# Performance work log

Hardware: AMD Instinct MI355X
Metric: run time of the kernel (lower is better)

Reference implementation:

```python
import jax, jax.numpy as jnp
import numpy as np
from jax import lax

B, T, V, E, H, K = 64, 512, 30000, 256, 256, 9


def setup_inputs() -> dict:
    key = jax.random.key(0)
    ks = jax.random.split(key, 15)
    s = 0.08
    return {
        "word_inputs": jax.random.randint(ks[0], (B, T), 0, V),
        "word_seq_lengths": jax.random.randint(ks[1], (B,), 1, T + 1),
        "seq_token_label": jax.random.randint(ks[2], (B, T), 0, K),
        "word_vec": jax.random.normal(ks[3], (V, E), jnp.float32) * s,
        "W_ih_f": jax.random.normal(ks[4], (4 * H, E), jnp.float32) * s,
        "W_hh_f": jax.random.normal(ks[5], (4 * H, H), jnp.float32) * s,
        "b_f": jax.random.normal(ks[6], (4 * H,), jnp.float32) * s,
        "W_ih_b": jax.random.normal(ks[7], (4 * H, E), jnp.float32) * s,
        "W_hh_b": jax.random.normal(ks[8], (4 * H, H), jnp.float32) * s,
        "b_b": jax.random.normal(ks[9], (4 * H,), jnp.float32) * s,
        "W_out": jax.random.normal(ks[10], (K, 2 * H), jnp.float32) * s,
        "b_out": jax.random.normal(ks[11], (K,), jnp.float32) * s,
        "start_trans": jax.random.normal(ks[12], (K,), jnp.float32) * s,
        "end_trans": jax.random.normal(ks[13], (K,), jnp.float32) * s,
        "trans": jax.random.normal(ks[14], (K, K), jnp.float32) * s,
    }


def _lstm_dir(x, W_ih, W_hh, b):
    # x: [B,T,E] -> h: [B,T,H]; torch gate order (i, f, g, o)
    gx = jnp.einsum('bte,ge->btg', x, W_ih) + b  # input projection hoisted out of scan
    h0 = jnp.zeros((x.shape[0], W_hh.shape[1]), x.dtype)

    def step(carry, g_t):
        h, c = carry
        g = g_t + h @ W_hh.T
        i, f, gg, o = jnp.split(g, 4, axis=-1)
        c = jax.nn.sigmoid(f) * c + jax.nn.sigmoid(i) * jnp.tanh(gg)
        h = jax.nn.sigmoid(o) * jnp.tanh(c)
        return (h, c), h

    _, hs = lax.scan(step, (h0, h0), jnp.swapaxes(gx, 0, 1))
    return jnp.swapaxes(hs, 0, 1)


def reference(word_inputs, word_seq_lengths, seq_token_label, word_vec,
              W_ih_f, W_hh_f, b_f, W_ih_b, W_hh_b, b_b,
              W_out, b_out, start_trans, end_trans, trans):
    t_idx = jnp.arange(T)
    mask = t_idx[None, :] < word_seq_lengths[:, None]  # [B,T] bool (pack_padded semantics)
    # index map that reverses the valid prefix of each sequence (involution)
    rev_idx = jnp.where(mask, word_seq_lengths[:, None] - 1 - t_idx[None, :], t_idx[None, :])

    emb = word_vec[word_inputs]  # [B,T,E]
    h_fwd = _lstm_dir(emb, W_ih_f, W_hh_f, b_f)
    emb_rev = jnp.take_along_axis(emb, rev_idx[:, :, None], axis=1)
    h_bwd = jnp.take_along_axis(_lstm_dir(emb_rev, W_ih_b, W_hh_b, b_b), rev_idx[:, :, None], axis=1)
    feats = jnp.concatenate([h_fwd, h_bwd], axis=-1) * mask[:, :, None]  # [B,T,2H]
    emissions = feats @ W_out.T + b_out  # [B,T,K]

    mf = mask.astype(emissions.dtype)
    # ---- CRF numerator (score of gold path) ----
    emit_sc = jnp.take_along_axis(emissions, seq_token_label[:, :, None], 2)[:, :, 0]  # [B,T]
    num = start_trans[seq_token_label[:, 0]] + emit_sc[:, 0]
    trans_sc = trans[seq_token_label[:, :-1], seq_token_label[:, 1:]]  # [B,T-1]
    num = num + jnp.sum((trans_sc + emit_sc[:, 1:]) * mf[:, 1:], axis=1)
    last_tags = jnp.take_along_axis(seq_token_label, (word_seq_lengths - 1)[:, None], 1)[:, 0]
    num = num + end_trans[last_tags]

    # ---- CRF log-partition (alpha recursion) ----
    em_t = jnp.swapaxes(emissions[:, 1:], 0, 1)  # [T-1,B,K]
    mk_t = jnp.swapaxes(mask[:, 1:], 0, 1)       # [T-1,B]
    score0 = start_trans[None, :] + emissions[:, 0]  # [B,K]

    def alpha_step(score, inp):
        e_t, m_t = inp
        nxt = jax.nn.logsumexp(score[:, :, None] + trans[None], axis=1) + e_t
        return jnp.where(m_t[:, None], nxt, score), None

    scoreZ, _ = lax.scan(alpha_step, score0, (em_t, mk_t))
    denom = jax.nn.logsumexp(scoreZ + end_trans[None, :], axis=1)
    ner_loss = -jnp.mean(num - denom)  # reduction='mean' over batch, negated

    # ---- Viterbi decode ----
    def vit_step(score, inp):
        e_t, m_t = inp
        tot = score[:, :, None] + trans[None]  # [B,K,K]
        best_prev = jnp.argmax(tot, axis=1)    # [B,K]
        nxt = jnp.max(tot, axis=1) + e_t
        return jnp.where(m_t[:, None], nxt, score), best_prev

    scoreV, hist = lax.scan(vit_step, score0, (em_t, mk_t))  # hist [T-1,B,K]
    best_last = jnp.argmax(scoreV + end_trans[None, :], axis=1)  # [B]

    def back_step(cur, inp):
        h_t, m_t = inp
        new = jnp.take_along_axis(h_t, cur[:, None], 1)[:, 0]
        cur = jnp.where(m_t, new, cur)
        return cur, cur

    _, preds_rev = lax.scan(back_step, best_last, (hist[::-1], mk_t[::-1]))  # [T-1,B]
    preds = jnp.concatenate([jnp.swapaxes(preds_rev[::-1], 0, 1), best_last[:, None]], axis=1)  # [B,T]
    preds = jnp.where(mask, preds, 0)

    return ner_loss, preds, feats
```

## Files before the change

kernel.cpp:

```cpp
#include <hip/hip_runtime.h>
#include <hip/hip_bf16.h>
#include <math.h>

#ifndef __has_builtin
#define __has_builtin(x) 0
#endif

typedef unsigned int uint;
typedef unsigned short ushort;
typedef _Float16 half2_t __attribute__((ext_vector_type(2)));


__device__ __forceinline__ float sigm(float x) {
    return __fdividef(1.0f, 1.0f + __expf(-x));
}
__device__ __forceinline__ float tanh_fast(float x) {
    float sg = __fdividef(1.0f, 1.0f + __expf(-2.0f * x));
    return sg + sg - 1.0f;
}
__device__ __forceinline__ float dot2f(uint w, uint h, float acc) {
#if __has_builtin(__builtin_amdgcn_fdot2)
    return __builtin_amdgcn_fdot2(__builtin_bit_cast(half2_t, w),
                                  __builtin_bit_cast(half2_t, h), acc, false);
#else
    half2_t a = __builtin_bit_cast(half2_t, w);
    half2_t b = __builtin_bit_cast(half2_t, h);
    return acc + (float)a.x * (float)b.x + (float)a.y * (float)b.y;
#endif
}

__global__ __launch_bounds__(256) void zero_kernel(float* __restrict__ out,
                                                   const int* __restrict__ lens) {
    int bid = blockIdx.x;
    if (bid < 65536) {
        int g = bid * 256 + threadIdx.x;
        int row = g >> 9;
        int t = row & 511;
        int b = row >> 9;
        if (t >= lens[b]) out[32769 + g] = 0.0f;
    } else if (bid < 65536 + 128) {
        int p = (bid - 65536) * 256 + threadIdx.x;
        out[1 + p] = 0.0f;
    } else if (threadIdx.x == 0) {
        out[0] = 0.0f;
    }
}

__global__ __launch_bounds__(256) void pack_kernel(const float* __restrict__ WF,
                                                   const float* __restrict__ WB,
                                                   uint* __restrict__ wregF,
                                                   uint* __restrict__ wregB,
                                                   uint* __restrict__ wldsF,
                                                   uint* __restrict__ wldsB) {
    int id = blockIdx.x * 256 + threadIdx.x;
    const float* W = WF; uint* wr = wregF; uint* wl = wldsF;
    if (id >= 131072) { id -= 131072; W = WB; wr = wregB; wl = wldsB; }
    int tl = id & 511;
    int x  = (id >> 9) & 1;
    int m  = id >> 10;
    int j = tl >> 1, s = tl & 1;
    int q = (s << 1) + x;
    float f0 = W[(((q << 8) + j) << 8) + 2 * m];
    float f1 = W[(((q << 8) + j) << 8) + 2 * m + 1];
    ushort u0 = __builtin_bit_cast(ushort, (_Float16)f0);
    ushort u1 = __builtin_bit_cast(ushort, (_Float16)f1);
    uint pk = (uint)u0 | ((uint)u1 << 16);
    if (m < 96) wr[((m << 1) + x) * 512 + tl];
    if (m < 96) wr[((m << 1) + x) * 512 + tl] = pk;
    else        wl[((m - 96) << 10) + (tl << 1) + x] = pk;
}

__global__ __launch_bounds__(256) void gemm_gx_kernel(const int* __restrict__ widx,
                                                      const int* __restrict__ lens,
                                                      const float* __restrict__ wvec,
                                                      const float* __restrict__ Wih,
                                                      const float* __restrict__ bias,
                                                      _Float16* __restrict__ gx) {
    int row0 = blockIdx.x * 64;
    int b = row0 >> 9;
    int t0 = row0 & 511;
    if (t0 >= lens[b]) return;
    int n0 = blockIdx.y * 64;

    __shared__ __align__(16) float As[16][68];
    __shared__ __align__(16) float Bs[16][68];
    __shared__ int aoff[64];

    int tid = threadIdx.x;
    if (tid < 64) aoff[tid] = widx[row0 + tid] << 8;
    __syncthreads();

    float acc[4][4] = {};
    int tn = tid & 15, tm = tid >> 4;

    for (int k0 = 0; k0 < 256; k0 += 16) {
#pragma unroll
        for (int p = 0; p < 4; ++p) {
            int lin = p * 256 + tid;
            int k = lin & 15, m = lin >> 4;
            int col = n0 + m;
            int perm = ((col & 3) << 8) + (col >> 2);
            As[k][m] = wvec[aoff[m] + k0 + k];
            Bs[k][m] = Wih[(perm << 8) + k0 + k];
        }
        __syncthreads();
#pragma unroll
        for (int k = 0; k < 16; ++k) {
            float4 av = *reinterpret_cast<const float4*>(&As[k][tm * 4]);
            float4 bv = *reinterpret_cast<const float4*>(&Bs[k][tn * 4]);
            float am[4] = {av.x, av.y, av.z, av.w};
            float bn[4] = {bv.x, bv.y, bv.z, bv.w};
#pragma unroll
            for (int i = 0; i < 4; ++i)
#pragma unroll
                for (int j = 0; j < 4; ++j) acc[i][j] = fmaf(am[i], bn[j], acc[i][j]);
        }
        __syncthreads();
    }

#pragma unroll
    for (int i = 0; i < 4; ++i) {
        int row = row0 + tm * 4 + i;
        ushort u[4];
#pragma unroll
        for (int j = 0; j < 4; ++j) {
            int col = n0 + tn * 4 + j;
            int perm = ((col & 3) << 8) + (col >> 2);
            u[j] = __builtin_bit_cast(ushort, (_Float16)(acc[i][j] + bias[perm]));
        }
        uint2 st;
        st.x = (uint)u[0] | ((uint)u[1] << 16);
        st.y = (uint)u[2] | ((uint)u[3] << 16);
        *reinterpret_cast<uint2*>(&gx[row * 1024 + n0 + tn * 4]) = st;
    }
}

__global__ __launch_bounds__(512, 2) void lstm_kernel(const _Float16* __restrict__ gx0,
                                                      const _Float16* __restrict__ gx1,
                                                      const uint* __restrict__ wreg0,
                                                      const uint* __restrict__ wreg1,
                                                      const uint* __restrict__ wlds0,
                                                      const uint* __restrict__ wlds1,
                                                      const int* __restrict__ lens,
                                                      float* __restrict__ feats) {
    int dir = blockIdx.x & 1;
    int b = blockIdx.x >> 1;
    const uint* gxu = reinterpret_cast<const uint*>(dir ? gx1 : gx0) + ((size_t)(b << 9) << 9);
    const uint* wreg = dir ? wreg1 : wreg0;
    const uint* wlds = dir ? wlds1 : wlds0;
    int len = lens[b];
    int tid = threadIdx.x;
    int lane = tid & 63;
    int sg = tid & 1;

    __shared__ __align__(16) uint lw[32 * 1024];
    __shared__ __align__(16) uint hpair[2][128];

    for (int i = tid; i < 32768; i += 512) lw[i] = wlds[i];

    uint wA[96], wB[96];
#pragma unroll
    for (int m = 0; m < 96; ++m) {
        wA[m] = wreg[((m << 1) + 0) * 512 + tid];
        wB[m] = wreg[((m << 1) + 1) * 512 + tid];
    }
    __syncthreads();

    float c = 0.0f;
    uint r0 = 0, r1 = 0;
    int pp = 0;

    int t0i = dir ? (len - 1) : 0;
    uint g = gxu[(t0i << 9) + tid];

    for (int tp = 0; tp < len; ++tp) {
        int t = dir ? (len - 1 - tp) : tp;
        int tnn = dir ? (len - 2 - tp) : (tp + 1);
        tnn = tnn < 0 ? 0 : (tnn >= len ? len - 1 : tnn);
        uint gnext = gxu[(tnn << 9) + tid];

        half2_t gv = __builtin_bit_cast(half2_t, g);
        float aA = (float)gv.x;
        float aB = (float)gv.y;

#pragma unroll
        for (int m = 0; m < 96; ++m) {
            uint hp = (uint)__builtin_amdgcn_readlane((int)(m < 64 ? r0 : r1), m & 63);
            aA = dot2f(wA[m], hp, aA);
            aB = dot2f(wB[m], hp, aB);
        }
#pragma unroll
        for (int i = 0; i < 32; ++i) {
            uint hp = (uint)__builtin_amdgcn_readlane((int)r1, 32 + i);
            uint2 w = reinterpret_cast<const uint2*>(lw)[(i << 9) + tid];
            aA = dot2f(w.x, hp, aA);
            aB = dot2f(w.y, hp, aB);
        }

        float y = sg ? aA + aA : aA;
        float sgm = __fdividef(1.0f, 1.0f + __expf(-y));
        float pA = sg ? sgm + sgm - 1.0f : sgm;
        float pB = sigm(aB);

        float oA = __shfl_xor(pA, 1);
        float oB = __shfl_xor(pB, 1);
        float si = sg ? oA : pA;
        float sf = sg ? oB : pB;
        float tg = sg ? pA : oA;
        float so = sg ? pB : oB;

        c = sf * c + si * tg;
        float h = so * tanh_fast(c);

        if (!sg) {
            reinterpret_cast<ushort*>(hpair[pp])[tid >> 1] =
                __builtin_bit_cast(ushort, (_Float16)h);
            feats[(size_t)(((b << 9) + t)) * 512 + (dir << 8) + (tid >> 1)] = h;
        }
        __syncthreads();
        r0 = hpair[pp][lane];
        r1 = hpair[pp][64 + lane];
        pp ^= 1;
        g = gnext;
    }
}

__global__ __launch_bounds__(64) void emis_kernel(const float* __restrict__ feats,
                                                  const float* __restrict__ Wout,
                                                  const float* __restrict__ bout,
                                                  const int* __restrict__ lens,
                                                  float* __restrict__ emis) {
    int r = blockIdx.x;
    int b = r >> 9, t = r & 511;
    if (t >= lens[b]) return;
    int lane = threadIdx.x;
    const float* fr = feats + (size_t)r * 512;
    float f[8];
#pragma unroll
    for (int i = 0; i < 8; ++i) f[i] = fr[i * 64 + lane];
#pragma unroll
    for (int k = 0; k < 9; ++k) {
        float p = 0.0f;
#pragma unroll
        for (int i = 0; i < 8; ++i) p = fmaf(f[i], Wout[k * 512 + i * 64 + lane], p);
#pragma unroll
        for (int off = 32; off; off >>= 1) p += __shfl_down(p, off);
        if (lane == 0) emis[r * 9 + k] = p + bout[k];
    }
}

__global__ __launch_bounds__(64) void crf_kernel(const float* __restrict__ emis,
                                                 const int* __restrict__ lens,
                                                 const int* __restrict__ labels,
                                                 const float* __restrict__ start_trans,
                                                 const float* __restrict__ end_trans,
                                                 const float* __restrict__ trans,
                                                 float* __restrict__ out) {
    int b = blockIdx.x;
    int len = lens[b];
    int lane = threadIdx.x;
    __shared__ float alpha[9], vit[9];
    __shared__ unsigned char hist[512 * 9];
    const float* eb = emis + b * 512 * 9;
    const int* lb = labels + b * 512;

    float tr[9];
    if (lane < 9) {
#pragma unroll
        for (int i = 0; i < 9; ++i) tr[i] = trans[i * 9 + lane];
        float s0 = start_trans[lane] + eb[lane];
        alpha[lane] = s0;
        vit[lane] = s0;
    }
    __syncthreads();

    for (int t = 1; t < len; ++t) {
        float na = 0.0f, nv = 0.0f;
        if (lane < 9) {
            float e = eb[t * 9 + lane];
            float a[9];
#pragma unroll
            for (int i = 0; i < 9; ++i) a[i] = alpha[i] + tr[i];
            float m = a[0];
#pragma unroll
            for (int i = 1; i < 9; ++i) m = fmaxf(m, a[i]);
            float s = 0.0f;
#pragma unroll
            for (int i = 0; i < 9; ++i) s += __expf(a[i] - m);
            na = m + __logf(s) + e;
            float bv = vit[0] + tr[0];
            int bi = 0;
#pragma unroll
            for (int i = 1; i < 9; ++i) {
                float x = vit[i] + tr[i];
                if (x > bv) { bv = x; bi = i; }
            }
            nv = bv + e;
            hist[t * 9 + lane] = (unsigned char)bi;
        }
        __syncthreads();
        if (lane < 9) { alpha[lane] = na; vit[lane] = nv; }
        __syncthreads();
    }

    float part = 0.0f;
    for (int t = 1 + lane; t < len; t += 64) {
        int yp = lb[t - 1], y = lb[t];
        part += trans[yp * 9 + y] + eb[t * 9 + y];
    }
#pragma unroll
    for (int off = 32; off; off >>= 1) part += __shfl_down(part, off);

    if (lane == 0) {
        int y0 = lb[0];
        float num = start_trans[y0] + eb[y0] + part + end_trans[lb[len - 1]];
        float m = alpha[0] + end_trans[0];
        for (int j = 1; j < 9; ++j) m = fmaxf(m, alpha[j] + end_trans[j]);
        float s = 0.0f;
        for (int j = 0; j < 9; ++j) s += __expf(alpha[j] + end_trans[j] - m);
        float denom = m + __logf(s);
        atomicAdd(out, (denom - num) * (1.0f / 64.0f));

        float bm = vit[0] + end_trans[0];
        int cur = 0;
        for (int j = 1; j < 9; ++j) {
            float x = vit[j] + end_trans[j];
            if (x > bm) { bm = x; cur = j; }
        }
        float* preds = out + 1 + b * 512;
        preds[len - 1] = (float)cur;
        for (int t = len - 1; t >= 1; --t) {
            cur = hist[t * 9 + cur];
            preds[t - 1] = (float)cur;
        }
    }
}

extern "C" void kernel_launch(void* const* d_in, const int* in_sizes, int n_in,
                              void* d_out, int out_size, void* d_ws, size_t ws_size,
                              hipStream_t stream) {
    const int* widx = (const int*)d_in[0];
    const int* lens = (const int*)d_in[1];
    const int* labels = (const int*)d_in[2];
    const float* wvec = (const float*)d_in[3];
    const float* WihF = (const float*)d_in[4];
    const float* WhhF = (const float*)d_in[5];
    const float* bF = (const float*)d_in[6];
    const float* WihB = (const float*)d_in[7];
    const float* WhhB = (const float*)d_in[8];
    const float* bB = (const float*)d_in[9];
    const float* Wout = (const float*)d_in[10];
    const float* bout = (const float*)d_in[11];
    const float* start_trans = (const float*)d_in[12];
    const float* end_trans = (const float*)d_in[13];
    const float* trans9 = (const float*)d_in[14];
    float* out = (float*)d_out;
    char* ws = (char*)d_ws;

    _Float16* gxF = (_Float16*)(ws);
    _Float16* gxB = (_Float16*)(ws + 67108864);
    uint* wregF   = (uint*)(ws + 134217728);
    uint* wregB   = (uint*)(ws + 134610944);
    uint* wldsF   = (uint*)(ws + 135004160);
    uint* wldsB   = (uint*)(ws + 135135232);
    float* emis   = (float*)(ws + 135266304);
    (void)in_sizes; (void)n_in; (void)out_size; (void)ws_size;

    float* feats = out + 1 + 32768;

    zero_kernel<<<65665, 256, 0, stream>>>(out, lens);
    pack_kernel<<<1024, 256, 0, stream>>>(WhhF, WhhB, wregF, wregB, wldsF, wldsB);

    dim3 ggrid(512, 16);
    gemm_gx_kernel<<<ggrid, 256, 0, stream>>>(widx, lens, wvec, WihF, bF, gxF);
    gemm_gx_kernel<<<ggrid, 256, 0, stream>>>(widx, lens, wvec, WihB, bB, gxB);

    lstm_kernel<<<128, 512, 0, stream>>>(gxF, gxB, wregF, wregB, wldsF, wldsB, lens, feats);

    emis_kernel<<<32768, 64, 0, stream>>>(feats, Wout, bout, lens, emis);
    crf_kernel<<<64, 64, 0, stream>>>(emis, lens, labels, start_trans, end_trans, trans9, out);
}
```

Measured before the change: 1.808 ms.

## Use fp16 dot2 in gx GEMM, rebalance LSTM register/LDS weight split

Pre-packs W_ih into fp16 pairs and rewrites the gx GEMM to accumulate with packed fp16 dot2 instructions. This halves the k-loop trips and the global loads per tile. In the LSTM recurrence, the register-resident weight columns drop from 96 to 90 and the LDS-resident part grows to 38 pairs. The LDS part is read with 128-bit loads covering two h pairs at once, which lowers register pressure and LDS instruction count. The risks are fp16 rounding of the embedding inputs in the GEMM and a wih16 workspace region that overlaps the emis buffer, though emis is written only after the GEMMs run.

```diff
diff --git a/kernel.cpp b/kernel.cpp
--- a/kernel.cpp
+++ b/kernel.cpp
@@ -10,6 +10,10 @@
 typedef unsigned short ushort;
 typedef _Float16 half2_t __attribute__((ext_vector_type(2)));
 
+#define PREG 90
+#define PLDS 38
+#define WREG_UINTS (PREG * 2 * 512)
+#define WLDS_UINTS (PLDS * 512 * 2)
 
 __device__ __forceinline__ float sigm(float x) {
     return __fdividef(1.0f, 1.0f + __expf(-x));
@@ -27,6 +31,11 @@
     half2_t b = __builtin_bit_cast(half2_t, h);
     return acc + (float)a.x * (float)b.x + (float)a.y * (float)b.y;
 #endif
+}
+__device__ __forceinline__ uint packh2(float a, float b) {
+    ushort u0 = __builtin_bit_cast(ushort, (_Float16)a);
+    ushort u1 = __builtin_bit_cast(ushort, (_Float16)b);
+    return (uint)u0 | ((uint)u1 << 16);
 }
 
 __global__ __launch_bounds__(256) void zero_kernel(float* __restrict__ out,
@@ -55,25 +64,48 @@
     int id = blockIdx.x * 256 + threadIdx.x;
     const float* W = WF; uint* wr = wregF; uint* wl = wldsF;
     if (id >= 131072) { id -= 131072; W = WB; wr = wregB; wl = wldsB; }
-    int tl = id & 511;
-    int x  = (id >> 9) & 1;
-    int m  = id >> 10;
+    int m, x, tl, dst_lds = 0, id2 = 0;
+    if (id < WREG_UINTS) {
+        m = id >> 10;
+        int r = id & 1023;
+        x = r >> 9;
+        tl = r & 511;
+    } else {
+        id2 = id - WREG_UINTS;
+        int c = id2 & 3;
+        int u = id2 >> 2;
+        tl = u & 511;
+        int g = u >> 9;
+        m = PREG + 2 * g + (c >> 1);
+        x = c & 1;
+        dst_lds = 1;
+    }
     int j = tl >> 1, s = tl & 1;
     int q = (s << 1) + x;
-    float f0 = W[(((q << 8) + j) << 8) + 2 * m];
-    float f1 = W[(((q << 8) + j) << 8) + 2 * m + 1];
-    ushort u0 = __builtin_bit_cast(ushort, (_Float16)f0);
-    ushort u1 = __builtin_bit_cast(ushort, (_Float16)f1);
-    uint pk = (uint)u0 | ((uint)u1 << 16);
-    if (m < 96) wr[((m << 1) + x) * 512 + tl];
-    if (m < 96) wr[((m << 1) + x) * 512 + tl] = pk;
-    else        wl[((m - 96) << 10) + (tl << 1) + x] = pk;
+    const float* row = W + ((size_t)((q << 8) + j) << 8);
+    uint pk = packh2(row[2 * m], row[2 * m + 1]);
+    if (dst_lds) wl[id2] = pk;
+    else         wr[((m << 1) + x) * 512 + tl] = pk;
+}
+
+__global__ __launch_bounds__(256) void wih_pack_kernel(const float* __restrict__ WihF,
+                                                       const float* __restrict__ WihB,
+                                                       uint* __restrict__ w16F,
+                                                       uint* __restrict__ w16B) {
+    int id = blockIdx.x * 256 + threadIdx.x;
+    const float* W = WihF; uint* dst = w16F;
+    if (id >= 131072) { id -= 131072; W = WihB; dst = w16B; }
+    int col = id >> 7;
+    int p = id & 127;
+    int perm = ((col & 3) << 8) + (col >> 2);
+    const float* row = W + ((size_t)perm << 8);
+    dst[(col << 7) + p] = packh2(row[2 * p], row[2 * p + 1]);
 }
 
 __global__ __launch_bounds__(256) void gemm_gx_kernel(const int* __restrict__ widx,
                                                       const int* __restrict__ lens,
                                                       const float* __restrict__ wvec,
-                                                      const float* __restrict__ Wih,
+                                                      const uint* __restrict__ wih16,
                                                       const float* __restrict__ bias,
                                                       _Float16* __restrict__ gx) {
     int row0 = blockIdx.x * 64;
@@ -82,8 +114,8 @@
     if (t0 >= lens[b]) return;
     int n0 = blockIdx.y * 64;
 
-    __shared__ __align__(16) float As[16][68];
-    __shared__ __align__(16) float Bs[16][68];
+    __shared__ __align__(16) uint As[16][68];
+    __shared__ __align__(16) uint Bs[16][68];
     __shared__ int aoff[64];
 
     int tid = threadIdx.x;
@@ -93,27 +125,27 @@
     float acc[4][4] = {};
     int tn = tid & 15, tm = tid >> 4;
 
-    for (int k0 = 0; k0 < 256; k0 += 16) {
+    for (int k0p = 0; k0p < 128; k0p += 16) {
 #pragma unroll
         for (int p = 0; p < 4; ++p) {
             int lin = p * 256 + tid;
-            int k = lin & 15, m = lin >> 4;
-            int col = n0 + m;
-            int perm = ((col & 3) << 8) + (col >> 2);
-            As[k][m] = wvec[aoff[m] + k0 + k];
-            Bs[k][m] = Wih[(perm << 8) + k0 + k];
+            int kp = lin & 15, m = lin >> 4;
+            const float2 av = *reinterpret_cast<const float2*>(
+                &wvec[aoff[m] + ((k0p + kp) << 1)]);
+            As[kp][m] = packh2(av.x, av.y);
+            Bs[kp][m] = wih16[((n0 + m) << 7) + k0p + kp];
         }
         __syncthreads();
 #pragma unroll
-        for (int k = 0; k < 16; ++k) {
-            float4 av = *reinterpret_cast<const float4*>(&As[k][tm * 4]);
-            float4 bv = *reinterpret_cast<const float4*>(&Bs[k][tn * 4]);
-            float am[4] = {av.x, av.y, av.z, av.w};
-            float bn[4] = {bv.x, bv.y, bv.z, bv.w};
+        for (int kp = 0; kp < 16; ++kp) {
+            uint4 a4 = *reinterpret_cast<const uint4*>(&As[kp][tm * 4]);
+            uint4 b4 = *reinterpret_cast<const uint4*>(&Bs[kp][tn * 4]);
+            uint am[4] = {a4.x, a4.y, a4.z, a4.w};
+            uint bn[4] = {b4.x, b4.y, b4.z, b4.w};
 #pragma unroll
             for (int i = 0; i < 4; ++i)
 #pragma unroll
-                for (int j = 0; j < 4; ++j) acc[i][j] = fmaf(am[i], bn[j], acc[i][j]);
+                for (int j = 0; j < 4; ++j) acc[i][j] = dot2f(am[i], bn[j], acc[i][j]);
         }
         __syncthreads();
     }
@@ -153,14 +185,14 @@
     int lane = tid & 63;
     int sg = tid & 1;
 
-    __shared__ __align__(16) uint lw[32 * 1024];
+    __shared__ __align__(16) uint lw[WLDS_UINTS];
     __shared__ __align__(16) uint hpair[2][128];
 
-    for (int i = tid; i < 32768; i += 512) lw[i] = wlds[i];
-
-    uint wA[96], wB[96];
-#pragma unroll
-    for (int m = 0; m < 96; ++m) {
+    for (int i = tid; i < WLDS_UINTS; i += 512) lw[i] = wlds[i];
+
+    uint wA[PREG], wB[PREG];
+#pragma unroll
+    for (int m = 0; m < PREG; ++m) {
         wA[m] = wreg[((m << 1) + 0) * 512 + tid];
         wB[m] = wreg[((m << 1) + 1) * 512 + tid];
     }
@@ -184,17 +216,20 @@
         float aB = (float)gv.y;
 
 #pragma unroll
-        for (int m = 0; m < 96; ++m) {
+        for (int m = 0; m < PREG; ++m) {
             uint hp = (uint)__builtin_amdgcn_readlane((int)(m < 64 ? r0 : r1), m & 63);
             aA = dot2f(wA[m], hp, aA);
             aB = dot2f(wB[m], hp, aB);
         }
 #pragma unroll
-        for (int i = 0; i < 32; ++i) {
-            uint hp = (uint)__builtin_amdgcn_readlane((int)r1, 32 + i);
-            uint2 w = reinterpret_cast<const uint2*>(lw)[(i << 9) + tid];
-            aA = dot2f(w.x, hp, aA);
-            aB = dot2f(w.y, hp, aB);
+        for (int i = 0; i < 19; ++i) {
+            uint4 w4 = reinterpret_cast<const uint4*>(lw)[(i << 9) + tid];
+            uint hp0 = (uint)__builtin_amdgcn_readlane((int)r1, 26 + 2 * i);
+            uint hp1 = (uint)__builtin_amdgcn_readlane((int)r1, 27 + 2 * i);
+            aA = dot2f(w4.x, hp0, aA);
+            aB = dot2f(w4.y, hp0, aB);
+            aA = dot2f(w4.z, hp1, aA);
+            aB = dot2f(w4.w, hp1, aB);
         }
 
         float y = sg ? aA + aA : aA;
@@ -360,9 +395,11 @@
     _Float16* gxF = (_Float16*)(ws);
     _Float16* gxB = (_Float16*)(ws + 67108864);
     uint* wregF   = (uint*)(ws + 134217728);
-    uint* wregB   = (uint*)(ws + 134610944);
-    uint* wldsF   = (uint*)(ws + 135004160);
-    uint* wldsB   = (uint*)(ws + 135135232);
+    uint* wregB   = (uint*)(ws + 134586368);
+    uint* wldsF   = (uint*)(ws + 134955008);
+    uint* wldsB   = (uint*)(ws + 135110656);
+    uint* wih16F  = (uint*)(ws + 135266304);
+    uint* wih16B  = (uint*)(ws + 135790592);
     float* emis   = (float*)(ws + 135266304);
     (void)in_sizes; (void)n_in; (void)out_size; (void)ws_size;
 
@@ -370,10 +407,11 @@
 
     zero_kernel<<<65665, 256, 0, stream>>>(out, lens);
     pack_kernel<<<1024, 256, 0, stream>>>(WhhF, WhhB, wregF, wregB, wldsF, wldsB);
+    wih_pack_kernel<<<1024, 256, 0, stream>>>(WihF, WihB, wih16F, wih16B);
 
     dim3 ggrid(512, 16);
-    gemm_gx_kernel<<<ggrid, 256, 0, stream>>>(widx, lens, wvec, WihF, bF, gxF);
-    gemm_gx_kernel<<<ggrid, 256, 0, stream>>>(widx, lens, wvec, WihB, bB, gxB);
+    gemm_gx_kernel<<<ggrid, 256, 0, stream>>>(widx, lens, wvec, wih16F, bF, gxF);
+    gemm_gx_kernel<<<ggrid, 256, 0, stream>>>(widx, lens, wvec, wih16B, bB, gxB);
 
     lstm_kernel<<<128, 512, 0, stream>>>(gxF, gxB, wregF, wregB, wldsF, wldsB, lens, feats);
 
```

Measured after the change: 1.652 ms. -8.6%, faster.
